# Kernel tuning notes

Measured on AMD Instinct MI355X. Metric: run time of the kernel, lower is better.

Reference implementation:

```python
import jax, jax.numpy as jnp
import numpy as np

# Module hyperparameters derived from init_kwargs
G = 100          # grid_size = int(n_samples ** gamma) = int(10000 ** 0.5)
K = 3            # KAN_SPLINE_ORDER
NB = G + K       # num_basis = 103
H = (1.5 - (-0.5)) / G
# grid identical for every input feature (torch expands a 1D grid)
GRID = jnp.arange(-K, G + K + 1, dtype=jnp.float32) * H - 0.5  # (G + 2K + 1,)


def bspline_basis(x):
    """Cox-de Boor recursion. x: (B, F) -> (B, F, NB)."""
    g = GRID
    xe = x[..., None]  # (B, F, 1)
    bases = ((xe >= g[:-1]) & (xe < g[1:])).astype(x.dtype)  # (B, F, G+2K)
    for k in range(1, K + 1):
        left = (xe - g[:-(k + 1)]) / jnp.maximum(g[k:-1] - g[:-(k + 1)], 1e-8)
        right = (g[k + 1:] - xe) / jnp.maximum(g[k + 1:] - g[1:-k], 1e-8)
        bases = left * bases[..., :-1] + right * bases[..., 1:]
    return bases  # (B, F, NB)


def kan_layer(x, bw, sw, wb, ws, residual):
    # base path: SiLU activation then linear
    base_out = jax.nn.silu(x) @ bw.T                      # (B, out)
    # spline path: basis expansion then contraction with spline_weight
    spline_out = jnp.einsum('bin,oin->bo', bspline_basis(x), sw)
    out = wb * base_out + ws * spline_out
    return out + x if residual else out


def setup_inputs() -> dict:
    key = jax.random.key(0)
    ks = jax.random.split(key, 16)
    B, D, W = 2048, 64, 243
    inp = {'x': jax.random.uniform(ks[0], (B, D), dtype=jnp.float32)}
    dims = [(D, W), (W, W), (W, W), (W, W), (W, W), (W, 1)]
    for i, (fi, fo) in enumerate(dims):
        kb, ksw = jax.random.split(jax.random.fold_in(key, i + 1))
        inp[f'bw{i}'] = jax.random.normal(kb, (fo, fi), dtype=jnp.float32) * (1.0 / np.sqrt(fi))
        # torch init: uniform(-0.5/G, 0.5/G)
        inp[f'sw{i}'] = jax.random.uniform(ksw, (fo, fi, NB), dtype=jnp.float32,
                                           minval=-0.5 / G, maxval=0.5 / G)
        inp[f'wb{i}'] = jnp.zeros((1,), dtype=jnp.float32)
        inp[f'ws{i}'] = jnp.ones((1,), dtype=jnp.float32)
    return inp


def reference(x, bw0, sw0, wb0, ws0, bw1, sw1, wb1, ws1, bw2, sw2, wb2, ws2,
              bw3, sw3, wb3, ws3, bw4, sw4, wb4, ws4, bw5, sw5, wb5, ws5):
    layers = [
        (bw0, sw0, wb0, ws0, False),  # 64 -> 243 (in != out: no residual)
        (bw1, sw1, wb1, ws1, True),
        (bw2, sw2, wb2, ws2, True),
        (bw3, sw3, wb3, ws3, True),
        (bw4, sw4, wb4, ws4, True),
        (bw5, sw5, wb5, ws5, False),  # 243 -> 1 (use_residual=False)
    ]
    h = x
    for bw, sw, wb, ws, res in layers:
        h = kan_layer(h, bw, sw, wb, ws, res)
    return h
```

## Files before the change

kernel.cpp:

```cpp
#include <hip/hip_runtime.h>
#include <hip/hip_fp16.h>
#include <math.h>

#define BATCH 2048
#define NBAS 103
#define NPAIR 102
#define OUTR 243
#define OUTP 256

typedef _Float16 half2v __attribute__((ext_vector_type(2)));

__device__ __forceinline__ float dot2(unsigned a, unsigned b, float c) {
#if __has_builtin(__builtin_amdgcn_fdot2)
    return __builtin_amdgcn_fdot2(__builtin_bit_cast(half2v, a),
                                  __builtin_bit_cast(half2v, b), c, false);
#else
    __half2 ha = __builtin_bit_cast(__half2, a), hb = __builtin_bit_cast(__half2, b);
    c = fmaf(__low2float(ha), __low2float(hb), c);
    c = fmaf(__high2float(ha), __high2float(hb), c);
    return c;
#endif
}

__device__ __forceinline__ uint4 make_meta(float x, int i) {
    float u = (x + 0.56f) * 50.0f;
    bool inr = (u >= 0.0f) && (u < 106.0f);
    float fj = floorf(u);
    float t = u - fj;
    int j = (int)fj;
    j = j < -1 ? -1 : (j > 106 ? 106 : j);
    float omt = 1.0f - t;
    float t2 = t * t, t3 = t2 * t;
    float w[4];
    w[0] = omt * omt * omt * (1.0f / 6.0f);
    w[1] = (3.0f * t3 - 6.0f * t2 + 4.0f) * (1.0f / 6.0f);
    w[2] = (-3.0f * t3 + 3.0f * t2 + 3.0f * t + 1.0f) * (1.0f / 6.0f);
    w[3] = t3 * (1.0f / 6.0f);
    int idx = j - 3;
    int idxc = idx < 0 ? 0 : (idx > 99 ? 99 : idx);
    int d = idx - idxc;
    float wc[4];
    #pragma unroll
    for (int m = 0; m < 4; ++m) {
        int s = m - d;
        wc[m] = (inr && s >= 0 && s < 4) ? w[s] : 0.0f;
    }
    __half2 w01 = __floats2half2_rn(wc[0], wc[1]);
    __half2 w23 = __floats2half2_rn(wc[2], wc[3]);
    uint4 m4;
    m4.x = __builtin_bit_cast(unsigned, w01);
    m4.y = __builtin_bit_cast(unsigned, w23);
    m4.z = (unsigned)((i * (NPAIR * 4) + idxc) << 6);
    m4.w = (unsigned)(i * NBAS + idxc);
    return m4;
}

__device__ __forceinline__ void pairgen_body64(
    const float* __restrict__ sw, int IN, unsigned* __restrict__ pairT,
    __half (*tile)[106], int i, int obase)
{
    int nl = threadIdx.x & 63;
    int w = threadIdx.x >> 6;
    #pragma unroll
    for (int k = 0; k < 16; ++k) {
        int r = w * 16 + k;
        int o = obase + r;
        if (o < OUTR) {
            const float* p = sw + ((size_t)o * IN + i) * NBAS;
            tile[r][nl] = __float2half(p[nl]);
            if (nl + 64 < NBAS)
                tile[r][nl + 64] = __float2half(p[nl + 64]);
        } else {
            tile[r][nl] = __ushort_as_half((unsigned short)0);
            if (nl + 64 < 106)
                tile[r][nl + 64] = __ushort_as_half((unsigned short)0);
        }
    }
    __syncthreads();
    int ol = threadIdx.x & 63;
    int rg = threadIdx.x >> 6;
    unsigned* dst = pairT + (size_t)i * (NPAIR * 4 * 64) + (size_t)(obase >> 6) * (NPAIR * 64);
    for (int r = 0; r < NPAIR; r += 4) {
        int rr = r + rg;
        if (rr < NPAIR) {
            unsigned lo = __half_as_ushort(tile[ol][rr]);
            unsigned hi = __half_as_ushort(tile[ol][rr + 1]);
            dst[(size_t)rr * 64 + ol] = lo | (hi << 16);
        }
    }
}

__device__ __forceinline__ void pairgen_body2i(
    const float* __restrict__ sw, int IN, unsigned* __restrict__ pairT,
    __half (*tile)[106], int i0, int obase, int ni)
{
    int nl = threadIdx.x & 63;
    int w = threadIdx.x >> 6;
    #pragma unroll
    for (int k = 0; k < 16; ++k) {
        int r = w * 16 + k;
        int o = obase + r;
        if (o < OUTR) {
            const float* p = sw + ((size_t)o * IN + i0) * NBAS;
            tile[r][nl] = __float2half(p[nl]);
            if (nl + 64 < NBAS)
                tile[r][nl + 64] = __float2half(p[nl + 64]);
            if (ni == 2) {
                tile[64 + r][nl] = __float2half(p[NBAS + nl]);
                if (nl + 64 < NBAS)
                    tile[64 + r][nl + 64] = __float2half(p[NBAS + nl + 64]);
            }
        } else {
            tile[r][nl] = __ushort_as_half((unsigned short)0);
            tile[64 + r][nl] = __ushort_as_half((unsigned short)0);
            if (nl + 64 < 106) {
                tile[r][nl + 64] = __ushort_as_half((unsigned short)0);
                tile[64 + r][nl + 64] = __ushort_as_half((unsigned short)0);
            }
        }
    }
    __syncthreads();
    int ol = threadIdx.x & 63;
    int rg = threadIdx.x >> 6;
    for (int q = 0; q < ni; ++q) {
        unsigned* dst = pairT + (size_t)(i0 + q) * (NPAIR * 4 * 64)
                              + (size_t)(obase >> 6) * (NPAIR * 64);
        const __half* trow = &tile[q * 64 + ol][0];
        for (int r = 0; r < NPAIR; r += 4) {
            int rr = r + rg;
            if (rr < NPAIR) {
                unsigned lo = __half_as_ushort(trow[rr]);
                unsigned hi = __half_as_ushort(trow[rr + 1]);
                dst[(size_t)rr * 64 + ol] = lo | (hi << 16);
            }
        }
    }
}

__global__ __launch_bounds__(256) void pairgen_kernel(
    const float* __restrict__ sw, int IN, unsigned* __restrict__ pairT)
{
    __shared__ __half tile[64][106];
    pairgen_body64(sw, IN, pairT, tile, blockIdx.x, blockIdx.y * 64);
}

__global__ __launch_bounds__(256) void pairgen_all_kernel(
    const float* __restrict__ sw0, const float* __restrict__ sw1,
    const float* __restrict__ sw2, const float* __restrict__ sw3,
    const float* __restrict__ sw4,
    unsigned* __restrict__ pT0, unsigned* __restrict__ pT1,
    unsigned* __restrict__ pT2, unsigned* __restrict__ pT3,
    unsigned* __restrict__ pT4,
    const float* __restrict__ xin, uint4* __restrict__ meta)
{
    __shared__ __half tile[128][106];
    int bx = blockIdx.x;
    if (bx < 2080) {
        const float* sw; unsigned* pt; int IN; int idx;
        if (bx < 128) { sw = sw0; pt = pT0; IN = 64; idx = bx; }
        else {
            int t = bx - 128;
            int l = t / 488;
            idx = t - l * 488;
            IN = OUTR;
            if (l == 0)      { sw = sw1; pt = pT1; }
            else if (l == 1) { sw = sw2; pt = pT2; }
            else if (l == 2) { sw = sw3; pt = pT3; }
            else             { sw = sw4; pt = pT4; }
        }
        int i0 = (idx >> 2) * 2;
        int ni = (i0 + 1 < IN) ? 2 : 1;
        pairgen_body2i(sw, IN, pt, tile, i0, (idx & 3) * 64, ni);
    } else {
        int e = (bx - 2080) * 256 + threadIdx.x;
        int b = e >> 6, i = e & 63;
        meta[e] = make_meta(xin[(size_t)b * 64 + i], i);
    }
}

template <int IN>
__global__ __launch_bounds__(256) void basis_kernel(
    const float* __restrict__ xin, int xstride, uint4* __restrict__ meta,
    float4* __restrict__ zbuf)
{
    int e = blockIdx.x * 256 + threadIdx.x;
    if (zbuf && e < (BATCH * OUTP) / 4) zbuf[e] = make_float4(0.f, 0.f, 0.f, 0.f);
    if (e >= BATCH * IN) return;
    int b = e / IN, i = e - b * IN;
    meta[e] = make_meta(xin[(size_t)b * xstride + i], i);
}

template <bool ADDRES>
__global__ __launch_bounds__(256) void basis_mid_kernel(
    const float* __restrict__ hprev,
    const float* __restrict__ parts,
    uint4* __restrict__ meta, float* __restrict__ hcomb)
{
    int e = blockIdx.x * 256 + threadIdx.x;
    if (e >= BATCH * OUTR) return;
    int b = e / OUTR, i = e - b * OUTR;
    size_t addr = (size_t)b * OUTP + i;
    const size_t PS = (size_t)BATCH * OUTP;
    float h = ADDRES ? hprev[addr] : 0.0f;
    #pragma unroll
    for (int s = 0; s < 8; ++s) h += parts[s * PS + addr];
    hcomb[addr] = h;
    meta[e] = make_meta(h, i);
}

template <bool ADDRES>
__global__ __launch_bounds__(256) void fused_pg_bm_kernel(
    const float* __restrict__ sw, unsigned* __restrict__ pairT,
    const float* __restrict__ hprev, const float* __restrict__ parts,
    uint4* __restrict__ meta, float* __restrict__ hcomb)
{
    if (blockIdx.y == 0) {
        __shared__ __half tile[64][106];
        if (blockIdx.x < 972)
            pairgen_body64(sw, OUTR, pairT, tile, blockIdx.x >> 2, (blockIdx.x & 3) * 64);
    } else {
        int e = blockIdx.x * 256 + threadIdx.x;
        if (e >= BATCH * OUTR) return;
        int b = e / OUTR, i = e - b * OUTR;
        size_t addr = (size_t)b * OUTP + i;
        const size_t PS = (size_t)BATCH * OUTP;
        float h = ADDRES ? hprev[addr] : 0.0f;
        #pragma unroll
        for (int s = 0; s < 8; ++s) h += parts[s * PS + addr];
        hcomb[addr] = h;
        meta[e] = make_meta(h, i);
    }
}

__global__ __launch_bounds__(256) void fused0_kernel(
    const float* __restrict__ sw0, unsigned* __restrict__ pairT,
    const float* __restrict__ xin, uint4* __restrict__ meta)
{
    if (blockIdx.y == 0) {
        __shared__ __half tile[64][106];
        if (blockIdx.x < 256)
            pairgen_body64(sw0, 64, pairT, tile, blockIdx.x >> 2, (blockIdx.x & 3) * 64);
    } else {
        int e = blockIdx.x * 256 + threadIdx.x;
        int b = e >> 6, i = e & 63;
        meta[e] = make_meta(xin[(size_t)b * 64 + i], i);
    }
}

template <int IN>
__global__ __launch_bounds__(256, 4) void layer_store_kernel(
    const unsigned* __restrict__ pairT, const uint4* __restrict__ meta,
    const float* __restrict__ h_in, int hstride,
    const float* __restrict__ bw,
    const float* __restrict__ wbp, const float* __restrict__ wsp,
    float* __restrict__ part)
{
    const int lane = threadIdx.x & 63;
    const int wave = __builtin_amdgcn_readfirstlane(threadIdx.x >> 6);
    const int b0 = blockIdx.y * 16 + wave * 4;
    const int cx = blockIdx.x;
    const int i0 = (IN * cx) >> 3;
    const int i1 = (IN * (cx + 1)) >> 3;
    const unsigned laneoff = ((unsigned)(lane >> 4) * (NPAIR * 64)) + ((unsigned)(lane & 15) << 2);
    const uint4* mp = meta + (size_t)b0 * IN;
    float a[4][4] = {};
    #pragma unroll 2
    for (int i = i0; i < i1; ++i) {
        uint4 m[4];
        #pragma unroll
        for (int r = 0; r < 4; ++r) m[r] = mp[(size_t)r * IN + i];
        uint4 lo[4], hi[4];
        #pragma unroll
        for (int r = 0; r < 4; ++r) {
            const uint4* p = (const uint4*)(pairT + m[r].z + laneoff);
            lo[r] = p[0];
            hi[r] = p[32];
        }
        #pragma unroll
        for (int r = 0; r < 4; ++r) {
            a[r][0] = dot2(m[r].x, lo[r].x, a[r][0]);
            a[r][1] = dot2(m[r].x, lo[r].y, a[r][1]);
            a[r][2] = dot2(m[r].x, lo[r].z, a[r][2]);
            a[r][3] = dot2(m[r].x, lo[r].w, a[r][3]);
            a[r][0] = dot2(m[r].y, hi[r].x, a[r][0]);
            a[r][1] = dot2(m[r].y, hi[r].y, a[r][1]);
            a[r][2] = dot2(m[r].y, hi[r].z, a[r][2]);
            a[r][3] = dot2(m[r].y, hi[r].w, a[r][3]);
        }
    }
    float wsv = wsp[0];
    float wbv = wbp[0];
    #pragma unroll
    for (int r = 0; r < 4; ++r) {
        float4 v = make_float4(wsv * a[r][0], wsv * a[r][1], wsv * a[r][2], wsv * a[r][3]);
        if (wbv != 0.0f) {
            float* pv = &v.x;
            for (int c = 0; c < 4; ++c) {
                int o = lane * 4 + c;
                if (o < OUTR) {
                    float bs = 0.0f;
                    for (int i = i0; i < i1; ++i) {
                        float xx = h_in[(size_t)(b0 + r) * hstride + i];
                        bs = fmaf(xx / (1.0f + expf(-xx)), bw[o * IN + i], bs);
                    }
                    pv[c] += wbv * bs;
                }
            }
        }
        float* d = part + ((size_t)cx * BATCH + b0 + r) * OUTP + lane * 4;
        *(float4*)d = v;
    }
}

template <int IN, bool RES>
__global__ __launch_bounds__(256, 8) void layer_atomic_kernel(
    const unsigned* __restrict__ pairT, const uint4* __restrict__ meta,
    const float* __restrict__ h_in, int hstride,
    const float* __restrict__ bw,
    const float* __restrict__ wbp, const float* __restrict__ wsp,
    float* __restrict__ out)
{
    const int lane = threadIdx.x & 63;
    const int wave = __builtin_amdgcn_readfirstlane(threadIdx.x >> 6);
    const int b = blockIdx.y * 4 + wave;
    const int cx = blockIdx.x;
    const int i0 = (IN * cx) >> 3;
    const int i1 = (IN * (cx + 1)) >> 3;
    const unsigned laneoff = ((unsigned)(lane >> 4) * (NPAIR * 64)) + ((unsigned)(lane & 15) << 2);
    const uint4* mp = meta + (size_t)b * IN;
    float acc[4] = {0.f, 0.f, 0.f, 0.f};
    #pragma unroll 2
    for (int i = i0; i < i1; ++i) {
        uint4 m = mp[i];
        const uint4* pA = (const uint4*)(pairT + m.z + laneoff);
        uint4 ra = pA[0];
        uint4 rb = pA[32];
        acc[0] = dot2(m.x, ra.x, acc[0]); acc[1] = dot2(m.x, ra.y, acc[1]);
        acc[2] = dot2(m.x, ra.z, acc[2]); acc[3] = dot2(m.x, ra.w, acc[3]);
        acc[0] = dot2(m.y, rb.x, acc[0]); acc[1] = dot2(m.y, rb.y, acc[1]);
        acc[2] = dot2(m.y, rb.z, acc[2]); acc[3] = dot2(m.y, rb.w, acc[3]);
    }
    float wsv = wsp[0];
    float wbv = wbp[0];
    #pragma unroll
    for (int c = 0; c < 4; ++c) {
        int o = lane * 4 + c;
        float v = wsv * acc[c];
        if (RES && cx == 0) v += h_in[(size_t)b * hstride + o];
        if (wbv != 0.0f && o < OUTR) {
            float bs = 0.0f;
            for (int i = i0; i < i1; ++i) {
                float xx = h_in[(size_t)b * hstride + i];
                bs = fmaf(xx / (1.0f + expf(-xx)), bw[o * IN + i], bs);
            }
            v += wbv * bs;
        }
        unsafeAtomicAdd(&out[(size_t)b * OUTP + o], v);
    }
}

__global__ __launch_bounds__(256) void final_fused_kernel(
    const float* __restrict__ sw5,
    const float* __restrict__ hprev,
    const float* __restrict__ parts,
    const float* __restrict__ bw5,
    const float* __restrict__ wbp, const float* __restrict__ wsp,
    float* __restrict__ out)
{
    int wave = threadIdx.x >> 6, lane = threadIdx.x & 63;
    int b = blockIdx.x * 4 + wave;
    const size_t PS = (size_t)BATCH * OUTP;
    float s = 0.0f, bs = 0.0f;
    for (int i = lane; i < OUTR; i += 64) {
        size_t addr = (size_t)b * OUTP + i;
        float h = hprev[addr];
        #pragma unroll
        for (int ss = 0; ss < 8; ++ss) h += parts[ss * PS + addr];
        uint4 m = make_meta(h, i);
        __half2 w01 = __builtin_bit_cast(__half2, m.x);
        __half2 w23 = __builtin_bit_cast(__half2, m.y);
        const float* p = sw5 + m.w;
        s += __low2float(w01) * p[0] + __high2float(w01) * p[1]
           + __low2float(w23) * p[2] + __high2float(w23) * p[3];
        bs = fmaf(h / (1.0f + expf(-h)), bw5[i], bs);
    }
    #pragma unroll
    for (int d = 32; d; d >>= 1) {
        s += __shfl_down(s, d, 64);
        bs += __shfl_down(bs, d, 64);
    }
    if (lane == 0) out[b] = wsp[0] * s + wbp[0] * bs;
}

__global__ __launch_bounds__(256) void final_kernel(
    const float* __restrict__ sw5,
    const uint4* __restrict__ meta,
    const float* __restrict__ h, const float* __restrict__ bw5,
    const float* __restrict__ wbp, const float* __restrict__ wsp,
    float* __restrict__ out)
{
    int wave = threadIdx.x >> 6, lane = threadIdx.x & 63;
    int b = blockIdx.x * 4 + wave;
    float s = 0.0f;
    for (int i = lane; i < OUTR; i += 64) {
        uint4 m = meta[(size_t)b * OUTR + i];
        __half2 w01 = __builtin_bit_cast(__half2, m.x);
        __half2 w23 = __builtin_bit_cast(__half2, m.y);
        const float* p = sw5 + m.w;
        s += __low2float(w01) * p[0] + __high2float(w01) * p[1]
           + __low2float(w23) * p[2] + __high2float(w23) * p[3];
    }
    #pragma unroll
    for (int d = 32; d; d >>= 1) s += __shfl_down(s, d, 64);
    if (lane == 0) {
        float v = wsp[0] * s;
        float wbv = wbp[0];
        if (wbv != 0.0f) {
            float bs = 0.0f;
            for (int i = 0; i < OUTR; ++i) {
                float xx = h[(size_t)b * OUTP + i];
                bs = fmaf(xx / (1.0f + expf(-xx)), bw5[i], bs);
            }
            v += wbv * bs;
        }
        out[b] = v;
    }
}

extern "C" void kernel_launch(void* const* d_in, const int* in_sizes, int n_in,
                              void* d_out, int out_size, void* d_ws, size_t ws_size,
                              hipStream_t stream)
{
    const float* x = (const float*)d_in[0];
    const float *bw[6], *sw[6], *wb[6], *ws[6];
    for (int l = 0; l < 6; ++l) {
        bw[l] = (const float*)d_in[1 + 4 * l];
        sw[l] = (const float*)d_in[2 + 4 * l];
        wb[l] = (const float*)d_in[3 + 4 * l];
        ws[l] = (const float*)d_in[4 + 4 * l];
    }
    char* base = (char*)d_ws;
    unsigned* pairT1 = (unsigned*)(base + 0);
    uint4*    meta   = (uint4*)(base + 25380864);
    float*    outp   = (float*)d_out;
    const int NB243 = (BATCH * OUTR + 255) / 256;

    const size_t NEED_ALL = 137142272;
    const size_t NEED_MID = 54315008;
    const size_t NEED_ATM = 37537792;

    if (ws_size >= NEED_ALL) {
        float*    parts  = (float*)(base + 33343488);
        float*    hcA    = (float*)(base + 50120704);
        float*    hcB    = (float*)(base + 52217856);
        unsigned* pairT0 = (unsigned*)(base + 54315008);
        unsigned* pairT2 = (unsigned*)(base + 60999680);
        unsigned* pairT3 = (unsigned*)(base + 86380544);
        unsigned* pairT4 = (unsigned*)(base + 111761408);
        unsigned* pT[5] = {pairT0, pairT1, pairT2, pairT3, pairT4};

        pairgen_all_kernel<<<2592, 256, 0, stream>>>(
            sw[0], sw[1], sw[2], sw[3], sw[4],
            pairT0, pairT1, pairT2, pairT3, pairT4, x, meta);

        layer_store_kernel<64><<<dim3(8, BATCH / 16), 256, 0, stream>>>(
            pairT0, meta, x, 64, bw[0], wb[0], ws[0], parts);

        float* hin = hcA; float* hout = hcB;
        for (int l = 1; l <= 4; ++l) {
            if (l == 1)
                basis_mid_kernel<false><<<NB243, 256, 0, stream>>>(nullptr, parts, meta, hin);
            else
                basis_mid_kernel<true><<<NB243, 256, 0, stream>>>(hout, parts, meta, hin);
            layer_store_kernel<243><<<dim3(8, BATCH / 16), 256, 0, stream>>>(
                pT[l], meta, hin, OUTP, bw[l], wb[l], ws[l], parts);
            float* tmp = hin; hin = hout; hout = tmp;
        }
        final_fused_kernel<<<BATCH / 4, 256, 0, stream>>>(
            sw[5], hout, parts, bw[5], wb[5], ws[5], outp);
    } else if (ws_size >= NEED_MID) {
        float* parts = (float*)(base + 33343488);
        float* hcA   = (float*)(base + 50120704);
        float* hcB   = (float*)(base + 52217856);

        fused0_kernel<<<dim3(512, 2), 256, 0, stream>>>(sw[0], pairT1, x, meta);
        layer_store_kernel<64><<<dim3(8, BATCH / 16), 256, 0, stream>>>(
            pairT1, meta, x, 64, bw[0], wb[0], ws[0], parts);

        float* hin = hcA; float* hout = hcB;
        for (int l = 1; l <= 4; ++l) {
            if (l == 1)
                fused_pg_bm_kernel<false><<<dim3(1944, 2), 256, 0, stream>>>(
                    sw[l], pairT1, nullptr, parts, meta, hin);
            else
                fused_pg_bm_kernel<true><<<dim3(1944, 2), 256, 0, stream>>>(
                    sw[l], pairT1, hout, parts, meta, hin);
            layer_store_kernel<243><<<dim3(8, BATCH / 16), 256, 0, stream>>>(
                pairT1, meta, hin, OUTP, bw[l], wb[l], ws[l], parts);
            float* tmp = hin; hin = hout; hout = tmp;
        }
        final_fused_kernel<<<BATCH / 4, 256, 0, stream>>>(
            sw[5], hout, parts, bw[5], wb[5], ws[5], outp);
    } else {
        if (ws_size < NEED_ATM) return;
        float* hA = (float*)(base + 33343488);
        float* hB = (float*)(base + 35440640);
        pairgen_kernel<<<dim3(64, 4), 256, 0, stream>>>(sw[0], 64, pairT1);
        basis_kernel<64><<<(BATCH * 64) / 256, 256, 0, stream>>>(x, 64, meta, (float4*)hA);
        layer_atomic_kernel<64, false><<<dim3(8, BATCH / 4), 256, 0, stream>>>(
            pairT1, meta, x, 64, bw[0], wb[0], ws[0], hA);
        float* hin = hA; float* hout = hB;
        for (int l = 1; l <= 4; ++l) {
            pairgen_kernel<<<dim3(OUTR, 4), 256, 0, stream>>>(sw[l], OUTR, pairT1);
            basis_kernel<243><<<NB243, 256, 0, stream>>>(hin, OUTP, meta, (float4*)hout);
            layer_atomic_kernel<243, true><<<dim3(8, BATCH / 4), 256, 0, stream>>>(
                pairT1, meta, hin, OUTP, bw[l], wb[l], ws[l], hout);
            float* tmp = hin; hin = hout; hout = tmp;
        }
        basis_kernel<243><<<NB243, 256, 0, stream>>>(hin, OUTP, meta, nullptr);
        final_kernel<<<BATCH / 4, 256, 0, stream>>>(sw[5], meta, hin, bw[5], wb[5], ws[5], outp);
    }
}
```

Measured before the change: 436.3 us.

## Overlap next-layer spline weight repacking with current layer compute

Instead of repacking all five spline-weight tensors up front in one large kernel, the front kernel now repacks only layers 0 and 1 along with the input metadata. Each middle layer's contraction kernel gets extra blocks that repack the next layer's weights concurrently. The aim is to hide weight conversion behind the memory-bound layer compute and shorten the serial front stage. The workspace layout is reshuffled so each layer keeps a separate packed buffer, and the extra blocks compete with the contraction for bandwidth and occupancy.

```diff
diff --git a/kernel.cpp b/kernel.cpp
--- a/kernel.cpp
+++ b/kernel.cpp
@@ -90,53 +90,6 @@
     }
 }
 
-__device__ __forceinline__ void pairgen_body2i(
-    const float* __restrict__ sw, int IN, unsigned* __restrict__ pairT,
-    __half (*tile)[106], int i0, int obase, int ni)
-{
-    int nl = threadIdx.x & 63;
-    int w = threadIdx.x >> 6;
-    #pragma unroll
-    for (int k = 0; k < 16; ++k) {
-        int r = w * 16 + k;
-        int o = obase + r;
-        if (o < OUTR) {
-            const float* p = sw + ((size_t)o * IN + i0) * NBAS;
-            tile[r][nl] = __float2half(p[nl]);
-            if (nl + 64 < NBAS)
-                tile[r][nl + 64] = __float2half(p[nl + 64]);
-            if (ni == 2) {
-                tile[64 + r][nl] = __float2half(p[NBAS + nl]);
-                if (nl + 64 < NBAS)
-                    tile[64 + r][nl + 64] = __float2half(p[NBAS + nl + 64]);
-            }
-        } else {
-            tile[r][nl] = __ushort_as_half((unsigned short)0);
-            tile[64 + r][nl] = __ushort_as_half((unsigned short)0);
-            if (nl + 64 < 106) {
-                tile[r][nl + 64] = __ushort_as_half((unsigned short)0);
-                tile[64 + r][nl + 64] = __ushort_as_half((unsigned short)0);
-            }
-        }
-    }
-    __syncthreads();
-    int ol = threadIdx.x & 63;
-    int rg = threadIdx.x >> 6;
-    for (int q = 0; q < ni; ++q) {
-        unsigned* dst = pairT + (size_t)(i0 + q) * (NPAIR * 4 * 64)
-                              + (size_t)(obase >> 6) * (NPAIR * 64);
-        const __half* trow = &tile[q * 64 + ol][0];
-        for (int r = 0; r < NPAIR; r += 4) {
-            int rr = r + rg;
-            if (rr < NPAIR) {
-                unsigned lo = __half_as_ushort(trow[rr]);
-                unsigned hi = __half_as_ushort(trow[rr + 1]);
-                dst[(size_t)rr * 64 + ol] = lo | (hi << 16);
-            }
-        }
-    }
-}
-
 __global__ __launch_bounds__(256) void pairgen_kernel(
     const float* __restrict__ sw, int IN, unsigned* __restrict__ pairT)
 {
@@ -144,35 +97,21 @@
     pairgen_body64(sw, IN, pairT, tile, blockIdx.x, blockIdx.y * 64);
 }
 
-__global__ __launch_bounds__(256) void pairgen_all_kernel(
-    const float* __restrict__ sw0, const float* __restrict__ sw1,
-    const float* __restrict__ sw2, const float* __restrict__ sw3,
-    const float* __restrict__ sw4,
-    unsigned* __restrict__ pT0, unsigned* __restrict__ pT1,
-    unsigned* __restrict__ pT2, unsigned* __restrict__ pT3,
-    unsigned* __restrict__ pT4,
+__global__ __launch_bounds__(256) void front_kernel(
+    const float* __restrict__ sw0, unsigned* __restrict__ pT0,
+    const float* __restrict__ sw1, unsigned* __restrict__ pT1,
     const float* __restrict__ xin, uint4* __restrict__ meta)
 {
-    __shared__ __half tile[128][106];
     int bx = blockIdx.x;
-    if (bx < 2080) {
-        const float* sw; unsigned* pt; int IN; int idx;
-        if (bx < 128) { sw = sw0; pt = pT0; IN = 64; idx = bx; }
+    if (bx < 1228) {
+        __shared__ __half tile[64][106];
+        if (bx < 256) pairgen_body64(sw0, 64, pT0, tile, bx >> 2, (bx & 3) * 64);
         else {
-            int t = bx - 128;
-            int l = t / 488;
-            idx = t - l * 488;
-            IN = OUTR;
-            if (l == 0)      { sw = sw1; pt = pT1; }
-            else if (l == 1) { sw = sw2; pt = pT2; }
-            else if (l == 2) { sw = sw3; pt = pT3; }
-            else             { sw = sw4; pt = pT4; }
-        }
-        int i0 = (idx >> 2) * 2;
-        int ni = (i0 + 1 < IN) ? 2 : 1;
-        pairgen_body2i(sw, IN, pt, tile, i0, (idx & 3) * 64, ni);
+            int t = bx - 256;
+            pairgen_body64(sw1, OUTR, pT1, tile, t >> 2, (t & 3) * 64);
+        }
     } else {
-        int e = (bx - 2080) * 256 + threadIdx.x;
+        int e = (bx - 1228) * 256 + threadIdx.x;
         int b = e >> 6, i = e & 63;
         meta[e] = make_meta(xin[(size_t)b * 64 + i], i);
     }
@@ -248,17 +187,16 @@
 }
 
 template <int IN>
-__global__ __launch_bounds__(256, 4) void layer_store_kernel(
+__device__ __forceinline__ void ls_body(
     const unsigned* __restrict__ pairT, const uint4* __restrict__ meta,
     const float* __restrict__ h_in, int hstride,
     const float* __restrict__ bw,
     const float* __restrict__ wbp, const float* __restrict__ wsp,
-    float* __restrict__ part)
+    float* __restrict__ part, int cx, int by)
 {
     const int lane = threadIdx.x & 63;
     const int wave = __builtin_amdgcn_readfirstlane(threadIdx.x >> 6);
-    const int b0 = blockIdx.y * 16 + wave * 4;
-    const int cx = blockIdx.x;
+    const int b0 = by * 16 + wave * 4;
     const int i0 = (IN * cx) >> 3;
     const int i1 = (IN * (cx + 1)) >> 3;
     const unsigned laneoff = ((unsigned)(lane >> 4) * (NPAIR * 64)) + ((unsigned)(lane & 15) << 2);
@@ -309,6 +247,36 @@
         }
         float* d = part + ((size_t)cx * BATCH + b0 + r) * OUTP + lane * 4;
         *(float4*)d = v;
+    }
+}
+
+template <int IN>
+__global__ __launch_bounds__(256, 4) void layer_store_kernel(
+    const unsigned* __restrict__ pairT, const uint4* __restrict__ meta,
+    const float* __restrict__ h_in, int hstride,
+    const float* __restrict__ bw,
+    const float* __restrict__ wbp, const float* __restrict__ wsp,
+    float* __restrict__ part)
+{
+    ls_body<IN>(pairT, meta, h_in, hstride, bw, wbp, wsp, part, blockIdx.x, blockIdx.y);
+}
+
+__global__ __launch_bounds__(256, 4) void ls_pg_kernel(
+    const unsigned* __restrict__ pairT, const uint4* __restrict__ meta,
+    const float* __restrict__ h_in, int hstride,
+    const float* __restrict__ bw,
+    const float* __restrict__ wbp, const float* __restrict__ wsp,
+    float* __restrict__ part,
+    const float* __restrict__ sw_next, unsigned* __restrict__ pT_next)
+{
+    if (blockIdx.x < 8) {
+        ls_body<OUTR>(pairT, meta, h_in, hstride, bw, wbp, wsp, part,
+                      blockIdx.x, blockIdx.y);
+    } else {
+        __shared__ __half tile[64][106];
+        int idx = (blockIdx.x - 8) + blockIdx.y * 8;
+        if (idx < 972)
+            pairgen_body64(sw_next, OUTR, pT_next, tile, idx >> 2, (idx & 3) * 64);
     }
 }
 
@@ -440,9 +408,7 @@
         ws[l] = (const float*)d_in[4 + 4 * l];
     }
     char* base = (char*)d_ws;
-    unsigned* pairT1 = (unsigned*)(base + 0);
-    uint4*    meta   = (uint4*)(base + 25380864);
-    float*    outp   = (float*)d_out;
+    float* outp = (float*)d_out;
     const int NB243 = (BATCH * OUTR + 255) / 256;
 
     const size_t NEED_ALL = 137142272;
@@ -450,21 +416,21 @@
     const size_t NEED_ATM = 37537792;
 
     if (ws_size >= NEED_ALL) {
-        float*    parts  = (float*)(base + 33343488);
-        float*    hcA    = (float*)(base + 50120704);
-        float*    hcB    = (float*)(base + 52217856);
-        unsigned* pairT0 = (unsigned*)(base + 54315008);
-        unsigned* pairT2 = (unsigned*)(base + 60999680);
-        unsigned* pairT3 = (unsigned*)(base + 86380544);
-        unsigned* pairT4 = (unsigned*)(base + 111761408);
-        unsigned* pT[5] = {pairT0, pairT1, pairT2, pairT3, pairT4};
-
-        pairgen_all_kernel<<<2592, 256, 0, stream>>>(
-            sw[0], sw[1], sw[2], sw[3], sw[4],
-            pairT0, pairT1, pairT2, pairT3, pairT4, x, meta);
+        unsigned* T0 = (unsigned*)(base + 0);
+        unsigned* T1 = (unsigned*)(base + 6684672);
+        unsigned* T2 = (unsigned*)(base + 32065536);
+        unsigned* T3 = (unsigned*)(base + 57446400);
+        unsigned* T4 = (unsigned*)(base + 82827264);
+        uint4*    meta  = (uint4*)(base + 108208128);
+        float*    parts = (float*)(base + 116170752);
+        float*    hcA   = (float*)(base + 132947968);
+        float*    hcB   = (float*)(base + 135045120);
+        unsigned* pT[5] = {T0, T1, T2, T3, T4};
+
+        front_kernel<<<1740, 256, 0, stream>>>(sw[0], T0, sw[1], T1, x, meta);
 
         layer_store_kernel<64><<<dim3(8, BATCH / 16), 256, 0, stream>>>(
-            pairT0, meta, x, 64, bw[0], wb[0], ws[0], parts);
+            T0, meta, x, 64, bw[0], wb[0], ws[0], parts);
 
         float* hin = hcA; float* hout = hcB;
         for (int l = 1; l <= 4; ++l) {
@@ -472,16 +438,23 @@
                 basis_mid_kernel<false><<<NB243, 256, 0, stream>>>(nullptr, parts, meta, hin);
             else
                 basis_mid_kernel<true><<<NB243, 256, 0, stream>>>(hout, parts, meta, hin);
-            layer_store_kernel<243><<<dim3(8, BATCH / 16), 256, 0, stream>>>(
-                pT[l], meta, hin, OUTP, bw[l], wb[l], ws[l], parts);
+            if (l <= 3)
+                ls_pg_kernel<<<dim3(16, BATCH / 16), 256, 0, stream>>>(
+                    pT[l], meta, hin, OUTP, bw[l], wb[l], ws[l], parts,
+                    sw[l + 1], pT[l + 1]);
+            else
+                layer_store_kernel<243><<<dim3(8, BATCH / 16), 256, 0, stream>>>(
+                    pT[4], meta, hin, OUTP, bw[4], wb[4], ws[4], parts);
             float* tmp = hin; hin = hout; hout = tmp;
         }
         final_fused_kernel<<<BATCH / 4, 256, 0, stream>>>(
             sw[5], hout, parts, bw[5], wb[5], ws[5], outp);
     } else if (ws_size >= NEED_MID) {
-        float* parts = (float*)(base + 33343488);
-        float* hcA   = (float*)(base + 50120704);
-        float* hcB   = (float*)(base + 52217856);
+        unsigned* pairT1 = (unsigned*)(base + 0);
+        uint4*    meta   = (uint4*)(base + 25380864);
+        float*    parts  = (float*)(base + 33343488);
+        float*    hcA    = (float*)(base + 50120704);
+        float*    hcB    = (float*)(base + 52217856);
 
         fused0_kernel<<<dim3(512, 2), 256, 0, stream>>>(sw[0], pairT1, x, meta);
         layer_store_kernel<64><<<dim3(8, BATCH / 16), 256, 0, stream>>>(
@@ -503,6 +476,8 @@
             sw[5], hout, parts, bw[5], wb[5], ws[5], outp);
     } else {
         if (ws_size < NEED_ATM) return;
+        unsigned* pairT1 = (unsigned*)(base + 0);
+        uint4*    meta   = (uint4*)(base + 25380864);
         float* hA = (float*)(base + 33343488);
         float* hB = (float*)(base + 35440640);
         pairgen_kernel<<<dim3(64, 4), 256, 0, stream>>>(sw[0], 64, pairT1);
```

Result: no change. 442.0 us (+1.3%).
